# Performance work log

Hardware: AMD Instinct MI355X
Metric: run time of the kernel (lower is better)

The kernel has to match this reference:

```python
import jax, jax.numpy as jnp
import numpy as np

B, S, DIM = 16, 1024, 1024
GAMMA = 0.96875
EPS = 1e-3  # keras GroupNormalization default epsilon


def setup_inputs() -> dict:
    key = jax.random.key(0)
    ks = jax.random.split(key, 4)
    scale = 1.0 / np.sqrt(DIM)
    return {
        "x": jax.random.normal(ks[0], (B, S, DIM), dtype=jnp.float32),
        "Wq": jax.random.normal(ks[1], (DIM, DIM), dtype=jnp.float32) * scale,
        "Wk": jax.random.normal(ks[2], (DIM, DIM), dtype=jnp.float32) * scale,
        "Wv": jax.random.normal(ks[3], (DIM, DIM), dtype=jnp.float32) * scale,
        "gn_scale": jnp.ones((DIM,), dtype=jnp.float32),
        "gn_beta": jnp.zeros((DIM,), dtype=jnp.float32),
    }


def reference(x, Wq, Wk, Wv, gn_scale, gn_beta):
    # Bias-free projections
    Q = x @ Wq  # [B,S,D]
    K = x @ Wk
    V = x @ Wv
    # Full (non-causal) exponential decay matrix D[i,j] = gamma^(i-j)
    idx = jnp.arange(S, dtype=jnp.float32)
    D = GAMMA ** (idx[:, None] - idx[None, :])  # [S,S]
    scores = jnp.einsum("bsd,btd->bst", Q, K) * D  # [B,S,S]
    y = scores @ V  # [B,S,D]
    # GroupNorm with groups == channels: normalize each channel over seq axis
    mean = jnp.mean(y, axis=1, keepdims=True)  # [B,1,D]
    var = jnp.var(y, axis=1, keepdims=True)
    y_hat = (y - mean) * jax.lax.rsqrt(var + EPS)
    return y_hat * gn_scale + gn_beta
```

## Files before the change

kernel.cpp:

```cpp
#include <hip/hip_runtime.h>
#include <cmath>

#define BATCH_ 16
#define SN_ 1024
#define DN_ 1024

constexpr float EPS_ = 1e-3f;

typedef unsigned short ushort;
typedef __attribute__((ext_vector_type(8))) short short8;
typedef __attribute__((ext_vector_type(8))) unsigned short ushort8;
typedef __attribute__((ext_vector_type(16))) float f32x16;

__device__ __forceinline__ ushort f2b(float f) {
    unsigned u = __float_as_uint(f);
    unsigned r = (u + 0x7fffu + ((u >> 16) & 1u)) >> 16;
    return (ushort)r;
}

__device__ __forceinline__ void gload16(const void* g, void* l) {
    __builtin_amdgcn_global_load_lds(
        (const __attribute__((address_space(1))) void*)g,
        (__attribute__((address_space(3))) void*)l, 16, 0, 0);
}

template<int MODE>
__global__ __launch_bounds__(512, 2)
void gemm_bf(const ushort* __restrict__ A0, const ushort* __restrict__ B0,
             void* __restrict__ C0, long sA, long sB, long sBm, long sC,
             float coef)
{
    constexpr bool TRANSP = (MODE == 2 || MODE == 3);
    constexpr bool SCALE  = (MODE == 1 || MODE == 3);

    __shared__ __align__(16) char lds[131072];

    const int gx = gridDim.x, gy = gridDim.y;
    int lid   = blockIdx.x + gx * (blockIdx.y + gy * blockIdx.z);
    int total = gx * gy * gridDim.z;
    int swz   = (lid & 7) * (total >> 3) + (lid >> 3);
    int bx = swz % gx;
    int rest = swz / gx;
    int by = rest % gy;
    int bz = rest / gy;

    const int m0 = by * 256, n0 = bx * 256;
    const ushort* A  = A0 + (long)bz * sA;
    const ushort* Bp = B0 + (long)bz * sB + (long)(m0 >> 10) * sBm;

    const int t = threadIdx.x;
    const int l = t & 63, w = t >> 6;
    const int wr = w >> 2, wc = w & 3;
    const int ln = l & 31;
    const int kb = l >> 5;
    const int lx = l & 7;

    const int aOff = (wr * 128 + ln) * 128;
    const int bOff = 32768 + (wc * 64 + ln) * 128;

    const int rl   = t >> 3;
    const int slot = (t & 7) ^ (rl & 7);
    const ushort* gA = A  + (long)(m0 + rl) * 1024 + slot * 8;
    const ushort* gB = Bp + (long)(n0 + rl) * 1024 + slot * 8;
    char* lA = lds + t * 16;
    char* lB = lds + 32768 + t * 16;

    f32x16 acc[4][2] = {};

#pragma unroll
    for (int h = 0; h < 4; ++h) {
        gload16(gA + (long)h * 64 * 1024, lA + h * 8192);
        gload16(gB + (long)h * 64 * 1024, lB + h * 8192);
    }
    __syncthreads();

    int buf = 0;
    for (int kt = 0; kt < 16; ++kt) {
        if (kt < 15) {
            int k0 = (kt + 1) * 64;
            int bo = (buf ^ 1) * 65536;
#pragma unroll
            for (int h = 0; h < 4; ++h) {
                gload16(gA + (long)h * 64 * 1024 + k0, lA + bo + h * 8192);
                gload16(gB + (long)h * 64 * 1024 + k0, lB + bo + h * 8192);
            }
        }
        const int bo = buf * 65536;
#pragma unroll
        for (int ks = 0; ks < 4; ++ks) {
            const int sx = ((ks * 2 + kb) ^ lx) * 16;
            short8 av[4], bv[2];
#pragma unroll
            for (int mi = 0; mi < 4; ++mi)
                av[mi] = *(const short8*)(lds + bo + aOff + mi * 4096 + sx);
#pragma unroll
            for (int nj = 0; nj < 2; ++nj)
                bv[nj] = *(const short8*)(lds + bo + bOff + nj * 4096 + sx);
            __builtin_amdgcn_s_setprio(1);
#pragma unroll
            for (int mi = 0; mi < 4; ++mi)
#pragma unroll
                for (int nj = 0; nj < 2; ++nj)
                    acc[mi][nj] = __builtin_amdgcn_mfma_f32_32x32x16_bf16(
                        av[mi], bv[nj], acc[mi][nj], 0, 0, 0);
            __builtin_amdgcn_s_setprio(0);
        }
        __syncthreads();
        buf ^= 1;
    }

    if constexpr (MODE == 0) {
        float* C = (float*)C0 + (long)bz * sC;
#pragma unroll
        for (int mi = 0; mi < 4; ++mi)
#pragma unroll
            for (int reg = 0; reg < 16; ++reg) {
                int row = m0 + wr * 128 + mi * 32 + (reg & 3) + 8 * (reg >> 2) + 4 * kb;
#pragma unroll
                for (int nj = 0; nj < 2; ++nj)
                    C[(long)row * 1024 + n0 + wc * 64 + nj * 32 + ln] =
                        acc[mi][nj][reg];
            }
    } else if constexpr (!TRANSP) {
        ushort* C = (ushort*)C0 + (long)bz * sC;
#pragma unroll
        for (int mi = 0; mi < 4; ++mi)
#pragma unroll
            for (int reg = 0; reg < 16; ++reg) {
                int row = m0 + wr * 128 + mi * 32 + (reg & 3) + 8 * (reg >> 2) + 4 * kb;
                float s = SCALE ? exp2f(coef * (float)(row & 1023)) : 1.0f;
#pragma unroll
                for (int nj = 0; nj < 2; ++nj)
                    C[(long)row * 1024 + n0 + wc * 64 + nj * 32 + ln] =
                        f2b(acc[mi][nj][reg] * s);
            }
    } else {
        ushort* Tl = (ushort*)lds;
        const int bb = m0 >> 10;
        const int ms = m0 & 1023;
        ushort* Ct = (ushort*)C0 + (long)bb * sC;
#pragma unroll
        for (int mi = 0; mi < 4; ++mi)
#pragma unroll
            for (int reg = 0; reg < 16; ++reg) {
                int rm = wr * 128 + mi * 32 + (reg & 3) + 8 * (reg >> 2) + 4 * kb;
                float s = SCALE ? exp2f(coef * (float)(ms + rm)) : 1.0f;
#pragma unroll
                for (int nj = 0; nj < 2; ++nj) {
                    int cn = wc * 64 + nj * 32 + ln;
                    int p  = (rm >> 3) ^ (cn & 31);
                    Tl[cn * 256 + p * 8 + (rm & 7)] = f2b(acc[mi][nj][reg] * s);
                }
            }
        __syncthreads();
#pragma unroll
        for (int it = 0; it < 16; ++it) {
            int cn = (t >> 5) + it * 16;
            int ch = t & 31;
            int p  = ch ^ (cn & 31);
            ushort8 v = *(const ushort8*)&Tl[cn * 256 + p * 8];
            *(ushort8*)&Ct[(long)(n0 + cn) * 1024 + ms + ch * 8] = v;
        }
    }
}

__global__ __launch_bounds__(256)
void conv_x_k(const float* __restrict__ x, ushort* __restrict__ xb)
{
    long i = ((long)blockIdx.x * 256 + threadIdx.x) * 8;
    float4 a = *(const float4*)&x[i];
    float4 b = *(const float4*)&x[i + 4];
    ushort8 v;
    v[0] = f2b(a.x); v[1] = f2b(a.y); v[2] = f2b(a.z); v[3] = f2b(a.w);
    v[4] = f2b(b.x); v[5] = f2b(b.y); v[6] = f2b(b.z); v[7] = f2b(b.w);
    *(ushort8*)&xb[i] = v;
}

__global__ __launch_bounds__(256)
void wt_k(const float* __restrict__ W, ushort* __restrict__ Wt)
{
    __shared__ float Tl[32][33];
    int tx = threadIdx.x & 31, ty = threadIdx.x >> 5;
    int c0 = blockIdx.x * 32, r0 = blockIdx.y * 32;
#pragma unroll
    for (int i = 0; i < 4; i++)
        Tl[ty + 8 * i][tx] = W[(long)(r0 + ty + 8 * i) * 1024 + c0 + tx];
    __syncthreads();
#pragma unroll
    for (int i = 0; i < 4; i++)
        Wt[(long)(c0 + ty + 8 * i) * 1024 + r0 + tx] = f2b(Tl[tx][ty + 8 * i]);
}

__global__ __launch_bounds__(256)
void stats1(const float* __restrict__ y, float* __restrict__ psum,
            float* __restrict__ psumsq)
{
    int d = blockIdx.x * 256 + threadIdx.x;
    int b = blockIdx.y;
    int z = blockIdx.z;
    const float* p = y + ((long)b * SN_ + (long)z * 128) * DN_ + d;
    float s = 0.f, ss = 0.f;
    for (int i = 0; i < 128; i++) {
        float v = p[(long)i * DN_];
        s += v;
        ss += v * v;
    }
    long o = ((long)z * BATCH_ + b) * DN_ + d;
    psum[o] = s;
    psumsq[o] = ss;
}

__global__ __launch_bounds__(256)
void stats2(const float* __restrict__ psum, const float* __restrict__ psumsq,
            const float* __restrict__ gsc, const float* __restrict__ gbt,
            float* __restrict__ fs, float* __restrict__ bias)
{
    int d = blockIdx.x * 256 + threadIdx.x;
    int b = blockIdx.y;
    float s = 0.f, ss = 0.f;
    for (int z = 0; z < 8; z++) {
        long o = ((long)z * BATCH_ + b) * DN_ + d;
        s += psum[o];
        ss += psumsq[o];
    }
    float mean = s * (1.0f / SN_);
    float var  = ss * (1.0f / SN_) - mean * mean;
    var = fmaxf(var, 0.0f);
    float rstd = rsqrtf(var + EPS_);
    float f = rstd * gsc[d];
    fs[(long)b * DN_ + d]   = f;
    bias[(long)b * DN_ + d] = gbt[d] - mean * f;
}

__global__ __launch_bounds__(256)
void norm_k(float* __restrict__ y, const float* __restrict__ fs,
            const float* __restrict__ bias)
{
    long i4 = (long)blockIdx.x * 256 + threadIdx.x;
    long e  = i4 * 4;
    int d = (int)(e & (DN_ - 1));
    int b = (int)(e >> 20);
    float4 v = *(float4*)&y[e];
    long o = (long)b * DN_ + d;
    float4 f  = *(const float4*)&fs[o];
    float4 bb = *(const float4*)&bias[o];
    v.x = v.x * f.x + bb.x;
    v.y = v.y * f.y + bb.y;
    v.z = v.z * f.z + bb.z;
    v.w = v.w * f.w + bb.w;
    *(float4*)&y[e] = v;
}

extern "C" void kernel_launch(void* const* d_in, const int* in_sizes, int n_in,
                              void* d_out, int out_size, void* d_ws, size_t ws_size,
                              hipStream_t stream)
{
    const float* x   = (const float*)d_in[0];
    const float* Wq  = (const float*)d_in[1];
    const float* Wk  = (const float*)d_in[2];
    const float* Wv  = (const float*)d_in[3];
    const float* gsc = (const float*)d_in[4];
    const float* gbt = (const float*)d_in[5];
    float* out = (float*)d_out;

    const long SD = (long)SN_ * DN_;
    const long DD = (long)DN_ * DN_;
    const size_t MB32 = (size_t)SD * BATCH_ * sizeof(ushort);

    char* ws = (char*)d_ws;
    ushort* xb  = (ushort*)(ws);
    ushort* Qp  = (ushort*)(ws + 1 * MB32);
    ushort* Kt  = (ushort*)(ws + 2 * MB32);
    ushort* Vt  = (ushort*)(ws + 3 * MB32);
    ushort* Mt  = (ushort*)(ws + 4 * MB32);
    ushort* Wtq = (ushort*)(ws + 5 * MB32);
    ushort* Wtk = (ushort*)(ws + 5 * MB32 + (2u << 20));
    ushort* Wtv = (ushort*)(ws + 5 * MB32 + (4u << 20));
    float*  psum   = (float*)(ws + 5 * MB32 + (6u << 20));
    float*  psumsq = (float*)(ws + 5 * MB32 + (6u << 20) + (1u << 19));
    float*  fs     = (float*)(ws + 5 * MB32 + (7u << 20));
    float*  bias   = (float*)(ws + 5 * MB32 + (7u << 20) + (1u << 18));

    const float lgf = (float)log2(0.96875);

    dim3 blk512(512);
    dim3 blk(256);
    dim3 gproj(4, 64);
    dim3 gmt(4, 4, 16);
    dim3 gy(4, 64);

    conv_x_k<<<dim3(8192), blk, 0, stream>>>(x, xb);
    wt_k<<<dim3(32, 32), blk, 0, stream>>>(Wq, Wtq);
    wt_k<<<dim3(32, 32), blk, 0, stream>>>(Wk, Wtk);
    wt_k<<<dim3(32, 32), blk, 0, stream>>>(Wv, Wtv);

    gemm_bf<1><<<gproj, blk512, 0, stream>>>(xb, Wtq, Qp, 0, 0, 0, 0, lgf);
    gemm_bf<3><<<gproj, blk512, 0, stream>>>(xb, Wtk, Kt, 0, 0, 0, SD, -lgf);
    gemm_bf<2><<<gproj, blk512, 0, stream>>>(xb, Wtv, Vt, 0, 0, 0, SD, 0.0f);
    gemm_bf<4><<<gmt, blk512, 0, stream>>>(Vt, Kt, Mt, SD, SD, 0, DD, 0.0f);
    gemm_bf<0><<<gy, blk512, 0, stream>>>(Qp, Mt, out, 0, 0, DD, 0, 0.0f);

    stats1<<<dim3(4, 16, 8), blk, 0, stream>>>(out, psum, psumsq);
    stats2<<<dim3(4, 16), blk, 0, stream>>>(psum, psumsq, gsc, gbt, fs, bias);
    norm_k<<<dim3(16384), blk, 0, stream>>>(out, fs, bias);
}
```

Before: 263.5 us.

## Fuse QKV projections, fuse GroupNorm stats into output GEMM, store bf16 intermediate

Merges the three projection GEMMs into one launch over a concatenated transposed weight matrix, with output routing done per column tile. The final GEMM now writes a bf16 result and accumulates per-channel partial sums and sums of squares in its epilogue, which removes the separate stats pass over the fp32 output. The norm kernel reads that bf16 buffer and writes fp32 output. The GEMM main loop is restructured to interleave the next tile's global-to-LDS loads with the MFMAs, using explicit waitcnt and scheduling barriers. Rounding the pre-norm output to bf16 adds some precision loss.

```diff
diff --git a/kernel.cpp b/kernel.cpp
--- a/kernel.cpp
+++ b/kernel.cpp
@@ -24,15 +24,16 @@
         (__attribute__((address_space(3))) void*)l, 16, 0, 0);
 }
 
+#define SCHED0 __builtin_amdgcn_sched_barrier(0)
+#define MFMA32(a, b, c) __builtin_amdgcn_mfma_f32_32x32x16_bf16(a, b, c, 0, 0, 0)
+
 template<int MODE>
 __global__ __launch_bounds__(512, 2)
 void gemm_bf(const ushort* __restrict__ A0, const ushort* __restrict__ B0,
-             void* __restrict__ C0, long sA, long sB, long sBm, long sC,
-             float coef)
-{
-    constexpr bool TRANSP = (MODE == 2 || MODE == 3);
-    constexpr bool SCALE  = (MODE == 1 || MODE == 3);
-
+             void* __restrict__ C0, void* __restrict__ C1, void* __restrict__ C2,
+             float* __restrict__ psum, float* __restrict__ psq,
+             long sA, long sB, long sBm, long sC, float coef)
+{
     __shared__ __align__(16) char lds[131072];
 
     const int gx = gridDim.x, gy = gridDim.y;
@@ -65,103 +66,148 @@
     char* lA = lds + t * 16;
     char* lB = lds + 32768 + t * 16;
 
+#define STA(h, k0, bo_) gload16(gA + (long)(h) * 65536 + (k0), lA + (bo_) + (h) * 8192)
+#define STB(h, k0, bo_) gload16(gB + (long)(h) * 65536 + (k0), lB + (bo_) + (h) * 8192)
+
     f32x16 acc[4][2] = {};
 
-#pragma unroll
-    for (int h = 0; h < 4; ++h) {
-        gload16(gA + (long)h * 64 * 1024, lA + h * 8192);
-        gload16(gB + (long)h * 64 * 1024, lB + h * 8192);
+    STB(0, 0, 0); STB(1, 0, 0); STB(2, 0, 0); STB(3, 0, 0);
+    STA(0, 0, 0); STA(1, 0, 0); STA(2, 0, 0); STA(3, 0, 0);
+    SCHED0;
+    asm volatile("s_waitcnt vmcnt(0)" ::: "memory");
+    SCHED0;
+    __builtin_amdgcn_s_barrier();
+    SCHED0;
+
+    for (int kt = 0; kt < 16; ++kt) {
+        const int bo = (kt & 1) << 16;
+        const int bn = bo ^ 65536;
+        const int k1 = (kt + 1) << 6;
+        const bool st = kt < 15;
+        const char* base = lds + bo;
+
+#pragma unroll
+        for (int p = 0; p < 4; ++p) {
+            const int sxp = ((p * 2 + kb) ^ lx) * 16;
+            short8 a0 = *(const short8*)(base + aOff + 0 * 4096 + sxp);
+            short8 a1 = *(const short8*)(base + aOff + 1 * 4096 + sxp);
+            short8 a2 = *(const short8*)(base + aOff + 2 * 4096 + sxp);
+            short8 a3 = *(const short8*)(base + aOff + 3 * 4096 + sxp);
+            short8 b0 = *(const short8*)(base + bOff + 0 * 4096 + sxp);
+            short8 b1 = *(const short8*)(base + bOff + 1 * 4096 + sxp);
+            if (st) {
+                if (p == 0) { STB(0, k1, bn); STB(1, k1, bn);
+                              STB(2, k1, bn); STB(3, k1, bn); }
+                else if (p == 1) { STA(0, k1, bn); STA(1, k1, bn);
+                                   STA(2, k1, bn); STA(3, k1, bn); }
+            }
+            __builtin_amdgcn_s_setprio(1);
+            acc[0][0] = MFMA32(a0, b0, acc[0][0]);
+            acc[0][1] = MFMA32(a0, b1, acc[0][1]);
+            acc[1][0] = MFMA32(a1, b0, acc[1][0]);
+            acc[1][1] = MFMA32(a1, b1, acc[1][1]);
+            acc[2][0] = MFMA32(a2, b0, acc[2][0]);
+            acc[2][1] = MFMA32(a2, b1, acc[2][1]);
+            acc[3][0] = MFMA32(a3, b0, acc[3][0]);
+            acc[3][1] = MFMA32(a3, b1, acc[3][1]);
+            __builtin_amdgcn_s_setprio(0);
+            SCHED0;
+        }
+        asm volatile("s_waitcnt vmcnt(0)" ::: "memory");
+        SCHED0;
+        __builtin_amdgcn_s_barrier();
+        SCHED0;
     }
-    __syncthreads();
-
-    int buf = 0;
-    for (int kt = 0; kt < 16; ++kt) {
-        if (kt < 15) {
-            int k0 = (kt + 1) * 64;
-            int bo = (buf ^ 1) * 65536;
-#pragma unroll
-            for (int h = 0; h < 4; ++h) {
-                gload16(gA + (long)h * 64 * 1024 + k0, lA + bo + h * 8192);
-                gload16(gB + (long)h * 64 * 1024 + k0, lB + bo + h * 8192);
+
+    if constexpr (MODE == 4) {
+        ushort* C = (ushort*)C0 + (long)bz * sC;
+#pragma unroll
+        for (int mi = 0; mi < 4; ++mi)
+#pragma unroll
+            for (int reg = 0; reg < 16; ++reg) {
+                int row = m0 + wr * 128 + mi * 32 + (reg & 3) + 8 * (reg >> 2) + 4 * kb;
+#pragma unroll
+                for (int nj = 0; nj < 2; ++nj)
+                    C[(long)row * 1024 + n0 + wc * 64 + nj * 32 + ln] =
+                        f2b(acc[mi][nj][reg]);
+            }
+    } else if constexpr (MODE == 5) {
+        ushort* C = (ushort*)C0;
+        float cs0 = 0.f, cq0 = 0.f, cs1 = 0.f, cq1 = 0.f;
+#pragma unroll
+        for (int mi = 0; mi < 4; ++mi)
+#pragma unroll
+            for (int reg = 0; reg < 16; ++reg) {
+                float v0 = acc[mi][0][reg], v1 = acc[mi][1][reg];
+                cs0 += v0; cq0 += v0 * v0;
+                cs1 += v1; cq1 += v1 * v1;
+                int row = m0 + wr * 128 + mi * 32 + (reg & 3) + 8 * (reg >> 2) + 4 * kb;
+                C[(long)row * 1024 + n0 + wc * 64 + ln]      = f2b(v0);
+                C[(long)row * 1024 + n0 + wc * 64 + 32 + ln] = f2b(v1);
+            }
+        float* S4 = (float*)lds;
+        float* Q4 = (float*)(lds + 4096);
+        {
+            int c0i = wc * 64 + ln, c1i = wc * 64 + 32 + ln, idx = wr * 2 + kb;
+            S4[c0i * 4 + idx] = cs0; S4[c1i * 4 + idx] = cs1;
+            Q4[c0i * 4 + idx] = cq0; Q4[c1i * 4 + idx] = cq1;
+        }
+        __syncthreads();
+        if (t < 256) {
+            float s = S4[t * 4] + S4[t * 4 + 1] + S4[t * 4 + 2] + S4[t * 4 + 3];
+            float q = Q4[t * 4] + Q4[t * 4 + 1] + Q4[t * 4 + 2] + Q4[t * 4 + 3];
+            psum[(long)by * 1024 + n0 + t] = s;
+            psq [(long)by * 1024 + n0 + t] = q;
+        }
+    } else {
+        const int which = n0 >> 10;
+        const int nq = n0 & 1023;
+        if (which == 0) {
+            ushort* C = (ushort*)C0;
+#pragma unroll
+            for (int mi = 0; mi < 4; ++mi)
+#pragma unroll
+                for (int reg = 0; reg < 16; ++reg) {
+                    int row = m0 + wr * 128 + mi * 32 + (reg & 3) + 8 * (reg >> 2) + 4 * kb;
+                    float s = exp2f(coef * (float)(row & 1023));
+#pragma unroll
+                    for (int nj = 0; nj < 2; ++nj)
+                        C[(long)row * 1024 + nq + wc * 64 + nj * 32 + ln] =
+                            f2b(acc[mi][nj][reg] * s);
+                }
+        } else {
+            ushort* Tl = (ushort*)lds;
+            const int bb = m0 >> 10;
+            const int ms = m0 & 1023;
+            ushort* Ct = (ushort*)((which == 1) ? C1 : C2) + (long)bb * sC;
+            const float cf = (which == 1) ? -coef : 0.0f;
+            __syncthreads();
+#pragma unroll
+            for (int mi = 0; mi < 4; ++mi)
+#pragma unroll
+                for (int reg = 0; reg < 16; ++reg) {
+                    int rm = wr * 128 + mi * 32 + (reg & 3) + 8 * (reg >> 2) + 4 * kb;
+                    float s = exp2f(cf * (float)(ms + rm));
+#pragma unroll
+                    for (int nj = 0; nj < 2; ++nj) {
+                        int cn = wc * 64 + nj * 32 + ln;
+                        int p  = (rm >> 3) ^ (cn & 31);
+                        Tl[cn * 256 + p * 8 + (rm & 7)] = f2b(acc[mi][nj][reg] * s);
+                    }
+                }
+            __syncthreads();
+#pragma unroll
+            for (int it = 0; it < 16; ++it) {
+                int cn = (t >> 5) + it * 16;
+                int ch = t & 31;
+                int p  = ch ^ (cn & 31);
+                ushort8 v = *(const ushort8*)&Tl[cn * 256 + p * 8];
+                *(ushort8*)&Ct[(long)(nq + cn) * 1024 + ms + ch * 8] = v;
             }
         }
-        const int bo = buf * 65536;
-#pragma unroll
-        for (int ks = 0; ks < 4; ++ks) {
-            const int sx = ((ks * 2 + kb) ^ lx) * 16;
-            short8 av[4], bv[2];
-#pragma unroll
-            for (int mi = 0; mi < 4; ++mi)
-                av[mi] = *(const short8*)(lds + bo + aOff + mi * 4096 + sx);
-#pragma unroll
-            for (int nj = 0; nj < 2; ++nj)
-                bv[nj] = *(const short8*)(lds + bo + bOff + nj * 4096 + sx);
-            __builtin_amdgcn_s_setprio(1);
-#pragma unroll
-            for (int mi = 0; mi < 4; ++mi)
-#pragma unroll
-                for (int nj = 0; nj < 2; ++nj)
-                    acc[mi][nj] = __builtin_amdgcn_mfma_f32_32x32x16_bf16(
-                        av[mi], bv[nj], acc[mi][nj], 0, 0, 0);
-            __builtin_amdgcn_s_setprio(0);
-        }
-        __syncthreads();
-        buf ^= 1;
     }
-
-    if constexpr (MODE == 0) {
-        float* C = (float*)C0 + (long)bz * sC;
-#pragma unroll
-        for (int mi = 0; mi < 4; ++mi)
-#pragma unroll
-            for (int reg = 0; reg < 16; ++reg) {
-                int row = m0 + wr * 128 + mi * 32 + (reg & 3) + 8 * (reg >> 2) + 4 * kb;
-#pragma unroll
-                for (int nj = 0; nj < 2; ++nj)
-                    C[(long)row * 1024 + n0 + wc * 64 + nj * 32 + ln] =
-                        acc[mi][nj][reg];
-            }
-    } else if constexpr (!TRANSP) {
-        ushort* C = (ushort*)C0 + (long)bz * sC;
-#pragma unroll
-        for (int mi = 0; mi < 4; ++mi)
-#pragma unroll
-            for (int reg = 0; reg < 16; ++reg) {
-                int row = m0 + wr * 128 + mi * 32 + (reg & 3) + 8 * (reg >> 2) + 4 * kb;
-                float s = SCALE ? exp2f(coef * (float)(row & 1023)) : 1.0f;
-#pragma unroll
-                for (int nj = 0; nj < 2; ++nj)
-                    C[(long)row * 1024 + n0 + wc * 64 + nj * 32 + ln] =
-                        f2b(acc[mi][nj][reg] * s);
-            }
-    } else {
-        ushort* Tl = (ushort*)lds;
-        const int bb = m0 >> 10;
-        const int ms = m0 & 1023;
-        ushort* Ct = (ushort*)C0 + (long)bb * sC;
-#pragma unroll
-        for (int mi = 0; mi < 4; ++mi)
-#pragma unroll
-            for (int reg = 0; reg < 16; ++reg) {
-                int rm = wr * 128 + mi * 32 + (reg & 3) + 8 * (reg >> 2) + 4 * kb;
-                float s = SCALE ? exp2f(coef * (float)(ms + rm)) : 1.0f;
-#pragma unroll
-                for (int nj = 0; nj < 2; ++nj) {
-                    int cn = wc * 64 + nj * 32 + ln;
-                    int p  = (rm >> 3) ^ (cn & 31);
-                    Tl[cn * 256 + p * 8 + (rm & 7)] = f2b(acc[mi][nj][reg] * s);
-                }
-            }
-        __syncthreads();
-#pragma unroll
-        for (int it = 0; it < 16; ++it) {
-            int cn = (t >> 5) + it * 16;
-            int ch = t & 31;
-            int p  = ch ^ (cn & 31);
-            ushort8 v = *(const ushort8*)&Tl[cn * 256 + p * 8];
-            *(ushort8*)&Ct[(long)(n0 + cn) * 1024 + ms + ch * 8] = v;
-        }
-    }
+#undef STA
+#undef STB
 }
 
 __global__ __launch_bounds__(256)
@@ -192,39 +238,21 @@
 }
 
 __global__ __launch_bounds__(256)
-void stats1(const float* __restrict__ y, float* __restrict__ psum,
-            float* __restrict__ psumsq)
+void stats2(const float* __restrict__ psum, const float* __restrict__ psq,
+            const float* __restrict__ gsc, const float* __restrict__ gbt,
+            float* __restrict__ fs, float* __restrict__ bias)
 {
     int d = blockIdx.x * 256 + threadIdx.x;
     int b = blockIdx.y;
-    int z = blockIdx.z;
-    const float* p = y + ((long)b * SN_ + (long)z * 128) * DN_ + d;
-    float s = 0.f, ss = 0.f;
-    for (int i = 0; i < 128; i++) {
-        float v = p[(long)i * DN_];
-        s += v;
-        ss += v * v;
-    }
-    long o = ((long)z * BATCH_ + b) * DN_ + d;
-    psum[o] = s;
-    psumsq[o] = ss;
-}
-
-__global__ __launch_bounds__(256)
-void stats2(const float* __restrict__ psum, const float* __restrict__ psumsq,
-            const float* __restrict__ gsc, const float* __restrict__ gbt,
-            float* __restrict__ fs, float* __restrict__ bias)
-{
-    int d = blockIdx.x * 256 + threadIdx.x;
-    int b = blockIdx.y;
-    float s = 0.f, ss = 0.f;
-    for (int z = 0; z < 8; z++) {
-        long o = ((long)z * BATCH_ + b) * DN_ + d;
+    float s = 0.f, q = 0.f;
+#pragma unroll
+    for (int z = 0; z < 4; z++) {
+        long o = ((long)(b * 4 + z) << 10) + d;
         s += psum[o];
-        ss += psumsq[o];
+        q += psq[o];
     }
     float mean = s * (1.0f / SN_);
-    float var  = ss * (1.0f / SN_) - mean * mean;
+    float var  = q * (1.0f / SN_) - mean * mean;
     var = fmaxf(var, 0.0f);
     float rstd = rsqrtf(var + EPS_);
     float f = rstd * gsc[d];
@@ -233,22 +261,29 @@
 }
 
 __global__ __launch_bounds__(256)
-void norm_k(float* __restrict__ y, const float* __restrict__ fs,
-            const float* __restrict__ bias)
-{
-    long i4 = (long)blockIdx.x * 256 + threadIdx.x;
-    long e  = i4 * 4;
-    int d = (int)(e & (DN_ - 1));
-    int b = (int)(e >> 20);
-    float4 v = *(float4*)&y[e];
+void norm_k(const ushort* __restrict__ yb, const float* __restrict__ fs,
+            const float* __restrict__ bias, float* __restrict__ out)
+{
+    long i = ((long)blockIdx.x * 256 + threadIdx.x) * 8;
+    int d = (int)(i & (DN_ - 1));
+    int b = (int)(i >> 20);
+    ushort8 v = *(const ushort8*)&yb[i];
     long o = (long)b * DN_ + d;
-    float4 f  = *(const float4*)&fs[o];
-    float4 bb = *(const float4*)&bias[o];
-    v.x = v.x * f.x + bb.x;
-    v.y = v.y * f.y + bb.y;
-    v.z = v.z * f.z + bb.z;
-    v.w = v.w * f.w + bb.w;
-    *(float4*)&y[e] = v;
+    float4 f0 = *(const float4*)&fs[o];
+    float4 f1 = *(const float4*)&fs[o + 4];
+    float4 b0 = *(const float4*)&bias[o];
+    float4 b1 = *(const float4*)&bias[o + 4];
+    float4 o0, o1;
+    o0.x = __uint_as_float((unsigned)v[0] << 16) * f0.x + b0.x;
+    o0.y = __uint_as_float((unsigned)v[1] << 16) * f0.y + b0.y;
+    o0.z = __uint_as_float((unsigned)v[2] << 16) * f0.z + b0.z;
+    o0.w = __uint_as_float((unsigned)v[3] << 16) * f0.w + b0.w;
+    o1.x = __uint_as_float((unsigned)v[4] << 16) * f1.x + b1.x;
+    o1.y = __uint_as_float((unsigned)v[5] << 16) * f1.y + b1.y;
+    o1.z = __uint_as_float((unsigned)v[6] << 16) * f1.z + b1.z;
+    o1.w = __uint_as_float((unsigned)v[7] << 16) * f1.w + b1.w;
+    *(float4*)&out[i]     = o0;
+    *(float4*)&out[i + 4] = o1;
 }
 
 extern "C" void kernel_launch(void* const* d_in, const int* in_sizes, int n_in,
@@ -273,34 +308,36 @@
     ushort* Kt  = (ushort*)(ws + 2 * MB32);
     ushort* Vt  = (ushort*)(ws + 3 * MB32);
     ushort* Mt  = (ushort*)(ws + 4 * MB32);
-    ushort* Wtq = (ushort*)(ws + 5 * MB32);
-    ushort* Wtk = (ushort*)(ws + 5 * MB32 + (2u << 20));
-    ushort* Wtv = (ushort*)(ws + 5 * MB32 + (4u << 20));
-    float*  psum   = (float*)(ws + 5 * MB32 + (6u << 20));
-    float*  psumsq = (float*)(ws + 5 * MB32 + (6u << 20) + (1u << 19));
-    float*  fs     = (float*)(ws + 5 * MB32 + (7u << 20));
-    float*  bias   = (float*)(ws + 5 * MB32 + (7u << 20) + (1u << 18));
+    ushort* Wct = (ushort*)(ws + 5 * MB32);
+    float*  psum = (float*)(ws + 5 * MB32 + (6u << 20));
+    float*  psq  = (float*)(ws + 5 * MB32 + (6u << 20) + (1u << 18));
+    float*  fs   = (float*)(ws + 5 * MB32 + (6u << 20) + (2u << 18));
+    float*  bias = (float*)(ws + 5 * MB32 + (6u << 20) + (2u << 18) + (1u << 16));
+    ushort* yb  = xb;
 
     const float lgf = (float)log2(0.96875);
 
     dim3 blk512(512);
     dim3 blk(256);
-    dim3 gproj(4, 64);
+    dim3 gproj(12, 64);
     dim3 gmt(4, 4, 16);
     dim3 gy(4, 64);
 
     conv_x_k<<<dim3(8192), blk, 0, stream>>>(x, xb);
-    wt_k<<<dim3(32, 32), blk, 0, stream>>>(Wq, Wtq);
-    wt_k<<<dim3(32, 32), blk, 0, stream>>>(Wk, Wtk);
-    wt_k<<<dim3(32, 32), blk, 0, stream>>>(Wv, Wtv);
-
-    gemm_bf<1><<<gproj, blk512, 0, stream>>>(xb, Wtq, Qp, 0, 0, 0, 0, lgf);
-    gemm_bf<3><<<gproj, blk512, 0, stream>>>(xb, Wtk, Kt, 0, 0, 0, SD, -lgf);
-    gemm_bf<2><<<gproj, blk512, 0, stream>>>(xb, Wtv, Vt, 0, 0, 0, SD, 0.0f);
-    gemm_bf<4><<<gmt, blk512, 0, stream>>>(Vt, Kt, Mt, SD, SD, 0, DD, 0.0f);
-    gemm_bf<0><<<gy, blk512, 0, stream>>>(Qp, Mt, out, 0, 0, DD, 0, 0.0f);
-
-    stats1<<<dim3(4, 16, 8), blk, 0, stream>>>(out, psum, psumsq);
-    stats2<<<dim3(4, 16), blk, 0, stream>>>(psum, psumsq, gsc, gbt, fs, bias);
-    norm_k<<<dim3(16384), blk, 0, stream>>>(out, fs, bias);
-}
+    wt_k<<<dim3(32, 32), blk, 0, stream>>>(Wq, Wct);
+    wt_k<<<dim3(32, 32), blk, 0, stream>>>(Wk, Wct + 1024 * 1024);
+    wt_k<<<dim3(32, 32), blk, 0, stream>>>(Wv, Wct + 2 * 1024 * 1024);
+
+    gemm_bf<6><<<gproj, blk512, 0, stream>>>(xb, Wct, Qp, Kt, Vt,
+                                             nullptr, nullptr,
+                                             0, 0, 0, SD, lgf);
+    gemm_bf<4><<<gmt, blk512, 0, stream>>>(Vt, Kt, Mt, nullptr, nullptr,
+                                           nullptr, nullptr,
+                                           SD, SD, 0, DD, 0.0f);
+    gemm_bf<5><<<gy, blk512, 0, stream>>>(Qp, Mt, yb, nullptr, nullptr,
+                                          psum, psq,
+                                          0, 0, DD, 0, 0.0f);
+
+    stats2<<<dim3(4, 16), blk, 0, stream>>>(psum, psq, gsc, gbt, fs, bias);
+    norm_k<<<dim3(8192), blk, 0, stream>>>(yb, fs, bias, out);
+}
```

Result: faster. 237.9 us (-9.7%).
